# Performance work log

Measured on AMD Instinct MI355X. Metric: run time of the kernel, lower is better.

Reference implementation:

```python
import jax, jax.numpy as jnp
import numpy as np

NEG_SLOPE = 0.01  # torch nn.LeakyReLU default


def setup_inputs() -> dict:
    key = jax.random.key(0)
    k1, k2, k3, k4 = jax.random.split(key, 4)
    N, D = 8192, 64
    x = jax.random.normal(k1, (N, D), dtype=jnp.float32)
    W = jax.random.normal(k2, (D, D), dtype=jnp.float32) * (1.0 / np.sqrt(D))
    b = jax.random.normal(k3, (D,), dtype=jnp.float32) * 0.01
    a = jax.random.normal(k4, (2 * D, 1), dtype=jnp.float32)
    return {"x": x, "W": W, "b": b, "a": a}


def reference(x, W, b, a):
    # h = Linear(x): torch stores weight as [out, in], y = x @ W.T + b
    h = x @ W.T + b  # [N, D]
    D = h.shape[1]
    a1 = a[:D, 0]   # weights on the column node (e_x[i,j] = x_j)
    a2 = a[D:, 0]   # weights on the row node    (e_y[i,j] = x_i)
    s1 = h @ a1     # [N], contribution of node j
    s2 = h @ a2     # [N], contribution of node i
    # score[i, j] = a1.h_j + a2.h_i  (equivalent to expand+concat+matmul)
    scores = s2[:, None] + s1[None, :]                       # [N, N]
    scores = jnp.where(scores >= 0, scores, NEG_SLOPE * scores)  # leaky_relu
    att = jax.nn.softmax(scores, axis=1)                     # softmax over j
    # NOTE: forward multiplies attention with the ORIGINAL x, not h
    return att @ x                                           # [N, D]
```

## Files before the change

### kernel.cpp

```cpp
#include <hip/hip_runtime.h>

#define NEG_SLOPE 0.01f
#define LOG2E 1.4426950408889634f

constexpr int N = 8192;
constexpr int D = 64;
constexpr int PB = 32;
constexpr int RB = 32;
constexpr int NW = 8;

typedef __bf16 bf16x8 __attribute__((ext_vector_type(8)));
typedef float f32x4 __attribute__((ext_vector_type(4)));

#if __has_builtin(__builtin_amdgcn_exp2f)
#define EXP2(x) __builtin_amdgcn_exp2f(x)
#else
#define EXP2(x) exp2f(x)
#endif

__global__ __launch_bounds__(256) void gat_prep(
    const float* __restrict__ x, const float* __restrict__ W_,
    const float* __restrict__ b, const float* __restrict__ a,
    float* __restrict__ s1g, float* __restrict__ s2g,
    float* __restrict__ blockmax, bf16x8* __restrict__ xf) {
  __shared__ float w1s[D], w2s[D], cs[2];
  __shared__ float s1loc[PB];

  const int t = threadIdx.x;
  const int bid = blockIdx.x;

  if (t < 128) {
    const int sel = t >> 6, d = t & 63;
    const float* av = a + sel * D;
    float acc = 0.f;
#pragma unroll
    for (int k = 0; k < D; ++k) acc += W_[k * D + d] * av[k];
    (sel ? w2s : w1s)[d] = acc * LOG2E;
  }
  if (t == 128 || t == 129) {
    const int sel = t - 128;
    float acc = 0.f;
    for (int d = 0; d < D; ++d) acc += b[d] * a[sel * D + d];
    cs[sel] = acc * LOG2E;
  }
  __syncthreads();

  {
    const int r = t >> 3, seg = t & 7;
    const int gi = bid * PB + r;
    const float4 xa = *(const float4*)(x + (size_t)gi * D + seg * 8);
    const float4 xb = *(const float4*)(x + (size_t)gi * D + seg * 8 + 4);
    float p1 = xa.x * w1s[seg * 8 + 0] + xa.y * w1s[seg * 8 + 1] +
               xa.z * w1s[seg * 8 + 2] + xa.w * w1s[seg * 8 + 3] +
               xb.x * w1s[seg * 8 + 4] + xb.y * w1s[seg * 8 + 5] +
               xb.z * w1s[seg * 8 + 6] + xb.w * w1s[seg * 8 + 7];
    float p2 = xa.x * w2s[seg * 8 + 0] + xa.y * w2s[seg * 8 + 1] +
               xa.z * w2s[seg * 8 + 2] + xa.w * w2s[seg * 8 + 3] +
               xb.x * w2s[seg * 8 + 4] + xb.y * w2s[seg * 8 + 5] +
               xb.z * w2s[seg * 8 + 6] + xb.w * w2s[seg * 8 + 7];
#pragma unroll
    for (int off = 4; off; off >>= 1) {
      p1 += __shfl_xor(p1, off, 64);
      p2 += __shfl_xor(p2, off, 64);
    }
    if (seg == 0) {
      const float v1 = p1 + cs[0], v2 = p2 + cs[1];
      s1g[gi] = v1;
      s2g[gi] = v2;
      s1loc[r] = v1;
    }
  }

  {
    const int dt = t >> 6, fl = t & 63;
    const int jb = bid * PB + ((fl >> 4) << 3);
    const int col = dt * 16 + (fl & 15);
    bf16x8 f;
#pragma unroll
    for (int q = 0; q < 8; ++q) f[q] = (__bf16)x[(size_t)(jb + q) * D + col];
    xf[(bid << 8) | (dt << 6) | fl] = f;
  }
  __syncthreads();
  if (t == 0) {
    float m = s1loc[0];
#pragma unroll
    for (int r = 1; r < PB; ++r) m = fmaxf(m, s1loc[r]);
    blockmax[bid] = m;
  }
}

__global__ __launch_bounds__(512, 2) void gat_main(
    const bf16x8* __restrict__ xf, const float* __restrict__ s1g,
    const float* __restrict__ s2g, const float* __restrict__ blockmax,
    float* __restrict__ out) {
  __shared__ float accT[NW][RB][64];
  __shared__ float zt[NW][RB];
  __shared__ float gms;

  const int t = threadIdx.x;
  const int lane = t & 63;
  const int w = t >> 6;
  const int arow = lane & 15;
  const int grp = lane >> 4;
  const int ibase = blockIdx.x * RB;

  if (t < 64) {
    float v = fmaxf(fmaxf(blockmax[lane], blockmax[lane + 64]),
                    fmaxf(blockmax[lane + 128], blockmax[lane + 192]));
#pragma unroll
    for (int off = 32; off; off >>= 1) v = fmaxf(v, __shfl_xor(v, off, 64));
    if (lane == 0) gms = v;
  }
  __syncthreads();
  const float gm = gms;

  const float s2v0 = s2g[ibase + arow];
  const float s2v1 = s2g[ibase + 16 + arow];
  const float tm0 = s2v0 + gm, tm1 = s2v1 + gm;
  const float mneg0 = -fmaxf(tm0, NEG_SLOPE * tm0);
  const float mneg1 = -fmaxf(tm1, NEG_SLOPE * tm1);

  f32x4 a00 = {0.f, 0.f, 0.f, 0.f}, a01 = a00, a02 = a00, a03 = a00;
  f32x4 a10 = a00, a11 = a00, a12 = a00, a13 = a00;
  f32x4 az0 = a00, az1 = a00;
  bf16x8 ones;
#pragma unroll
  for (int q = 0; q < 8; ++q) ones[q] = (__bf16)1.0f;

  int c = w;
  bf16x8 xb0 = xf[(c << 8) + 0 * 64 + lane];
  bf16x8 xb1 = xf[(c << 8) + 1 * 64 + lane];
  bf16x8 xb2 = xf[(c << 8) + 2 * 64 + lane];
  bf16x8 xb3 = xf[(c << 8) + 3 * 64 + lane];
  float4 sa = *(const float4*)(s1g + c * 32 + grp * 8);
  float4 sb = *(const float4*)(s1g + c * 32 + grp * 8 + 4);

  constexpr int ITERS = N / 32 / NW;
  for (int i = 0; i < ITERS; ++i) {
    const int cn = (i == ITERS - 1) ? c : c + NW;
    bf16x8 nb0 = xf[(cn << 8) + 0 * 64 + lane];
    bf16x8 nb1 = xf[(cn << 8) + 1 * 64 + lane];
    bf16x8 nb2 = xf[(cn << 8) + 2 * 64 + lane];
    bf16x8 nb3 = xf[(cn << 8) + 3 * 64 + lane];
    const float4 na = *(const float4*)(s1g + cn * 32 + grp * 8);
    const float4 nbb = *(const float4*)(s1g + cn * 32 + grp * 8 + 4);

    bf16x8 pa0, pa1;
    {
      const float* sv = &sa.x;
#pragma unroll
      for (int q = 0; q < 4; ++q) {
        const float t0 = s2v0 + sv[q];
        pa0[q] = (__bf16)EXP2(fmaxf(t0, NEG_SLOPE * t0) + mneg0);
        const float t1 = s2v1 + sv[q];
        pa1[q] = (__bf16)EXP2(fmaxf(t1, NEG_SLOPE * t1) + mneg1);
      }
      const float* sw = &sb.x;
#pragma unroll
      for (int q = 0; q < 4; ++q) {
        const float t0 = s2v0 + sw[q];
        pa0[4 + q] = (__bf16)EXP2(fmaxf(t0, NEG_SLOPE * t0) + mneg0);
        const float t1 = s2v1 + sw[q];
        pa1[4 + q] = (__bf16)EXP2(fmaxf(t1, NEG_SLOPE * t1) + mneg1);
      }
    }

    a00 = __builtin_amdgcn_mfma_f32_16x16x32_bf16(pa0, xb0, a00, 0, 0, 0);
    a01 = __builtin_amdgcn_mfma_f32_16x16x32_bf16(pa0, xb1, a01, 0, 0, 0);
    a02 = __builtin_amdgcn_mfma_f32_16x16x32_bf16(pa0, xb2, a02, 0, 0, 0);
    a03 = __builtin_amdgcn_mfma_f32_16x16x32_bf16(pa0, xb3, a03, 0, 0, 0);
    az0 = __builtin_amdgcn_mfma_f32_16x16x32_bf16(pa0, ones, az0, 0, 0, 0);
    a10 = __builtin_amdgcn_mfma_f32_16x16x32_bf16(pa1, xb0, a10, 0, 0, 0);
    a11 = __builtin_amdgcn_mfma_f32_16x16x32_bf16(pa1, xb1, a11, 0, 0, 0);
    a12 = __builtin_amdgcn_mfma_f32_16x16x32_bf16(pa1, xb2, a12, 0, 0, 0);
    a13 = __builtin_amdgcn_mfma_f32_16x16x32_bf16(pa1, xb3, a13, 0, 0, 0);
    az1 = __builtin_amdgcn_mfma_f32_16x16x32_bf16(pa1, ones, az1, 0, 0, 0);

    xb0 = nb0; xb1 = nb1; xb2 = nb2; xb3 = nb3;
    sa = na; sb = nbb;
    c += NW;
  }

  if (arow == 0) {
#pragma unroll
    for (int reg = 0; reg < 4; ++reg) {
      zt[w][grp * 4 + reg] = az0[reg];
      zt[w][16 + grp * 4 + reg] = az1[reg];
    }
  }

#pragma unroll
  for (int reg = 0; reg < 4; ++reg) {
    accT[w][grp * 4 + reg][0 * 16 + arow] = a00[reg];
    accT[w][grp * 4 + reg][1 * 16 + arow] = a01[reg];
    accT[w][grp * 4 + reg][2 * 16 + arow] = a02[reg];
    accT[w][grp * 4 + reg][3 * 16 + arow] = a03[reg];
    accT[w][16 + grp * 4 + reg][0 * 16 + arow] = a10[reg];
    accT[w][16 + grp * 4 + reg][1 * 16 + arow] = a11[reg];
    accT[w][16 + grp * 4 + reg][2 * 16 + arow] = a12[reg];
    accT[w][16 + grp * 4 + reg][3 * 16 + arow] = a13[reg];
  }
  __syncthreads();

#pragma unroll
  for (int k = 0; k < 4; ++k) {
    const int r = w * 4 + k;
    float s = 0.f, z = 0.f;
#pragma unroll
    for (int v = 0; v < NW; ++v) {
      s += accT[v][r][lane];
      z += zt[v][r];
    }
    out[(size_t)(ibase + r) * D + lane] = s / z;
  }
}

extern "C" void kernel_launch(void* const* d_in, const int* in_sizes, int n_in,
                              void* d_out, int out_size, void* d_ws, size_t ws_size,
                              hipStream_t stream) {
  const float* x = (const float*)d_in[0];
  const float* W = (const float*)d_in[1];
  const float* b = (const float*)d_in[2];
  const float* a = (const float*)d_in[3];

  float* s1 = (float*)d_ws;
  float* s2 = s1 + N;
  float* blockmax = s2 + N;
  bf16x8* xf = (bf16x8*)((char*)d_ws + (1u << 20));
  float* out = (float*)d_out;

  gat_prep<<<N / PB, 256, 0, stream>>>(x, W, b, a, s1, s2, blockmax, xf);
  gat_main<<<N / RB, 512, 0, stream>>>(xf, s1, s2, blockmax, out);
}
```

Baseline: 91.60 us.

## Fuse prep and main kernels into one, recomputing scores per block

Merges the two kernels into a single launch. Every block recomputes all N s1 scores into shared memory (32KB) and its own s2 rows, then takes the global max locally. The main loop now reads fp32 x directly with strided scalar loads and converts to bf16 in registers, instead of reading a prepacked bf16 layout. This removes a launch and the workspace round trip, but each of the 256 blocks redundantly reads all of x (2MB) for the score pass. It also adds register pressure from the 64-float prefetch buffers, uncoalesced loads and more shared memory per block.

```diff
diff --git a/kernel.cpp b/kernel.cpp
--- a/kernel.cpp
+++ b/kernel.cpp
@@ -5,29 +5,27 @@
 
 constexpr int N = 8192;
 constexpr int D = 64;
-constexpr int PB = 32;
 constexpr int RB = 32;
 constexpr int NW = 8;
 
 typedef __bf16 bf16x8 __attribute__((ext_vector_type(8)));
 typedef float f32x4 __attribute__((ext_vector_type(4)));
 
-#if __has_builtin(__builtin_amdgcn_exp2f)
-#define EXP2(x) __builtin_amdgcn_exp2f(x)
-#else
-#define EXP2(x) exp2f(x)
-#endif
-
-__global__ __launch_bounds__(256) void gat_prep(
+__global__ __launch_bounds__(512, 2) void gat_one(
     const float* __restrict__ x, const float* __restrict__ W_,
     const float* __restrict__ b, const float* __restrict__ a,
-    float* __restrict__ s1g, float* __restrict__ s2g,
-    float* __restrict__ blockmax, bf16x8* __restrict__ xf) {
+    float* __restrict__ out) {
   __shared__ float w1s[D], w2s[D], cs[2];
-  __shared__ float s1loc[PB];
+  __shared__ float s1All[N];
+  __shared__ float s2loc[RB];
+  __shared__ float wmax[NW];
+  __shared__ float accT[NW][RB][64];
+  __shared__ float zt[NW][RB];
 
   const int t = threadIdx.x;
   const int bid = blockIdx.x;
+  const int lane = t & 63;
+  const int w = t >> 6;
 
   if (t < 128) {
     const int sel = t >> 6, d = t & 63;
@@ -46,76 +44,53 @@
   __syncthreads();
 
   {
-    const int r = t >> 3, seg = t & 7;
-    const int gi = bid * PB + r;
-    const float4 xa = *(const float4*)(x + (size_t)gi * D + seg * 8);
-    const float4 xb = *(const float4*)(x + (size_t)gi * D + seg * 8 + 4);
-    float p1 = xa.x * w1s[seg * 8 + 0] + xa.y * w1s[seg * 8 + 1] +
-               xa.z * w1s[seg * 8 + 2] + xa.w * w1s[seg * 8 + 3] +
-               xb.x * w1s[seg * 8 + 4] + xb.y * w1s[seg * 8 + 5] +
-               xb.z * w1s[seg * 8 + 6] + xb.w * w1s[seg * 8 + 7];
-    float p2 = xa.x * w2s[seg * 8 + 0] + xa.y * w2s[seg * 8 + 1] +
-               xa.z * w2s[seg * 8 + 2] + xa.w * w2s[seg * 8 + 3] +
-               xb.x * w2s[seg * 8 + 4] + xb.y * w2s[seg * 8 + 5] +
-               xb.z * w2s[seg * 8 + 6] + xb.w * w2s[seg * 8 + 7];
-#pragma unroll
-    for (int off = 4; off; off >>= 1) {
-      p1 += __shfl_xor(p1, off, 64);
-      p2 += __shfl_xor(p2, off, 64);
-    }
-    if (seg == 0) {
-      const float v1 = p1 + cs[0], v2 = p2 + cs[1];
-      s1g[gi] = v1;
-      s2g[gi] = v2;
-      s1loc[r] = v1;
-    }
-  }
-
+    const int seg = t & 7;
+    const int rloc = t >> 3;
+    float w1r[8], w2r[8];
+#pragma unroll
+    for (int k = 0; k < 8; ++k) { w1r[k] = w1s[seg * 8 + k]; w2r[k] = w2s[seg * 8 + k]; }
+    const float c1 = cs[0], c2 = cs[1];
+#pragma unroll 4
+    for (int it = 0; it < N / 64; ++it) {
+      const int gi = it * 64 + rloc;
+      const float4 xa = *(const float4*)(x + (size_t)gi * D + seg * 8);
+      const float4 xb = *(const float4*)(x + (size_t)gi * D + seg * 8 + 4);
+      float p1 = xa.x * w1r[0] + xa.y * w1r[1] + xa.z * w1r[2] + xa.w * w1r[3] +
+                 xb.x * w1r[4] + xb.y * w1r[5] + xb.z * w1r[6] + xb.w * w1r[7];
+      float p2 = xa.x * w2r[0] + xa.y * w2r[1] + xa.z * w2r[2] + xa.w * w2r[3] +
+                 xb.x * w2r[4] + xb.y * w2r[5] + xb.z * w2r[6] + xb.w * w2r[7];
+#pragma unroll
+      for (int off = 1; off < 8; off <<= 1) {
+        p1 += __shfl_xor(p1, off, 64);
+        p2 += __shfl_xor(p2, off, 64);
+      }
+      if (seg == 0) {
+        s1All[gi] = p1 + c1;
+        const int rown = gi - bid * RB;
+        if ((unsigned)rown < (unsigned)RB) s2loc[rown] = p2 + c2;
+      }
+    }
+  }
+  __syncthreads();
+
+  float gm;
   {
-    const int dt = t >> 6, fl = t & 63;
-    const int jb = bid * PB + ((fl >> 4) << 3);
-    const int col = dt * 16 + (fl & 15);
-    bf16x8 f;
-#pragma unroll
-    for (int q = 0; q < 8; ++q) f[q] = (__bf16)x[(size_t)(jb + q) * D + col];
-    xf[(bid << 8) | (dt << 6) | fl] = f;
-  }
-  __syncthreads();
-  if (t == 0) {
-    float m = s1loc[0];
-#pragma unroll
-    for (int r = 1; r < PB; ++r) m = fmaxf(m, s1loc[r]);
-    blockmax[bid] = m;
-  }
-}
-
-__global__ __launch_bounds__(512, 2) void gat_main(
-    const bf16x8* __restrict__ xf, const float* __restrict__ s1g,
-    const float* __restrict__ s2g, const float* __restrict__ blockmax,
-    float* __restrict__ out) {
-  __shared__ float accT[NW][RB][64];
-  __shared__ float zt[NW][RB];
-  __shared__ float gms;
-
-  const int t = threadIdx.x;
-  const int lane = t & 63;
-  const int w = t >> 6;
+    float mv = -1e30f;
+#pragma unroll
+    for (int k = 0; k < N / 512; ++k) mv = fmaxf(mv, s1All[k * 512 + t]);
+#pragma unroll
+    for (int off = 32; off; off >>= 1) mv = fmaxf(mv, __shfl_xor(mv, off, 64));
+    if (lane == 0) wmax[w] = mv;
+    __syncthreads();
+    gm = wmax[0];
+#pragma unroll
+    for (int k = 1; k < NW; ++k) gm = fmaxf(gm, wmax[k]);
+  }
+
   const int arow = lane & 15;
   const int grp = lane >> 4;
-  const int ibase = blockIdx.x * RB;
-
-  if (t < 64) {
-    float v = fmaxf(fmaxf(blockmax[lane], blockmax[lane + 64]),
-                    fmaxf(blockmax[lane + 128], blockmax[lane + 192]));
-#pragma unroll
-    for (int off = 32; off; off >>= 1) v = fmaxf(v, __shfl_xor(v, off, 64));
-    if (lane == 0) gms = v;
-  }
-  __syncthreads();
-  const float gm = gms;
-
-  const float s2v0 = s2g[ibase + arow];
-  const float s2v1 = s2g[ibase + 16 + arow];
+  const float s2v0 = s2loc[arow];
+  const float s2v1 = s2loc[16 + arow];
   const float tm0 = s2v0 + gm, tm1 = s2v1 + gm;
   const float mneg0 = -fmaxf(tm0, NEG_SLOPE * tm0);
   const float mneg1 = -fmaxf(tm1, NEG_SLOPE * tm1);
@@ -127,23 +102,42 @@
 #pragma unroll
   for (int q = 0; q < 8; ++q) ones[q] = (__bf16)1.0f;
 
+  float xc[32], xn[32];
+  float4 sa, sb, na, nb;
+  {
+    const float* bp = x + (size_t)w * 2048 + grp * 512 + arow;
+#pragma unroll
+    for (int q = 0; q < 8; ++q)
+#pragma unroll
+      for (int dt = 0; dt < 4; ++dt) xc[q * 4 + dt] = bp[q * 64 + dt * 16];
+    const float* sp = &s1All[w * 32 + grp * 8];
+    sa = *(const float4*)sp;
+    sb = *(const float4*)(sp + 4);
+  }
+
+  constexpr int ITERS = N / 32 / NW;
   int c = w;
-  bf16x8 xb0 = xf[(c << 8) + 0 * 64 + lane];
-  bf16x8 xb1 = xf[(c << 8) + 1 * 64 + lane];
-  bf16x8 xb2 = xf[(c << 8) + 2 * 64 + lane];
-  bf16x8 xb3 = xf[(c << 8) + 3 * 64 + lane];
-  float4 sa = *(const float4*)(s1g + c * 32 + grp * 8);
-  float4 sb = *(const float4*)(s1g + c * 32 + grp * 8 + 4);
-
-  constexpr int ITERS = N / 32 / NW;
   for (int i = 0; i < ITERS; ++i) {
     const int cn = (i == ITERS - 1) ? c : c + NW;
-    bf16x8 nb0 = xf[(cn << 8) + 0 * 64 + lane];
-    bf16x8 nb1 = xf[(cn << 8) + 1 * 64 + lane];
-    bf16x8 nb2 = xf[(cn << 8) + 2 * 64 + lane];
-    bf16x8 nb3 = xf[(cn << 8) + 3 * 64 + lane];
-    const float4 na = *(const float4*)(s1g + cn * 32 + grp * 8);
-    const float4 nbb = *(const float4*)(s1g + cn * 32 + grp * 8 + 4);
+    {
+      const float* bp = x + (size_t)cn * 2048 + grp * 512 + arow;
+#pragma unroll
+      for (int q = 0; q < 8; ++q)
+#pragma unroll
+        for (int dt = 0; dt < 4; ++dt) xn[q * 4 + dt] = bp[q * 64 + dt * 16];
+      const float* sp = &s1All[cn * 32 + grp * 8];
+      na = *(const float4*)sp;
+      nb = *(const float4*)(sp + 4);
+    }
+
+    bf16x8 xb0, xb1, xb2, xb3;
+#pragma unroll
+    for (int q = 0; q < 8; ++q) {
+      xb0[q] = (__bf16)xc[q * 4 + 0];
+      xb1[q] = (__bf16)xc[q * 4 + 1];
+      xb2[q] = (__bf16)xc[q * 4 + 2];
+      xb3[q] = (__bf16)xc[q * 4 + 3];
+    }
 
     bf16x8 pa0, pa1;
     {
@@ -151,17 +145,17 @@
 #pragma unroll
       for (int q = 0; q < 4; ++q) {
         const float t0 = s2v0 + sv[q];
-        pa0[q] = (__bf16)EXP2(fmaxf(t0, NEG_SLOPE * t0) + mneg0);
+        pa0[q] = (__bf16)exp2f(fmaxf(t0, NEG_SLOPE * t0) + mneg0);
         const float t1 = s2v1 + sv[q];
-        pa1[q] = (__bf16)EXP2(fmaxf(t1, NEG_SLOPE * t1) + mneg1);
+        pa1[q] = (__bf16)exp2f(fmaxf(t1, NEG_SLOPE * t1) + mneg1);
       }
       const float* sw = &sb.x;
 #pragma unroll
       for (int q = 0; q < 4; ++q) {
         const float t0 = s2v0 + sw[q];
-        pa0[4 + q] = (__bf16)EXP2(fmaxf(t0, NEG_SLOPE * t0) + mneg0);
+        pa0[4 + q] = (__bf16)exp2f(fmaxf(t0, NEG_SLOPE * t0) + mneg0);
         const float t1 = s2v1 + sw[q];
-        pa1[4 + q] = (__bf16)EXP2(fmaxf(t1, NEG_SLOPE * t1) + mneg1);
+        pa1[4 + q] = (__bf16)exp2f(fmaxf(t1, NEG_SLOPE * t1) + mneg1);
       }
     }
 
@@ -176,8 +170,9 @@
     a13 = __builtin_amdgcn_mfma_f32_16x16x32_bf16(pa1, xb3, a13, 0, 0, 0);
     az1 = __builtin_amdgcn_mfma_f32_16x16x32_bf16(pa1, ones, az1, 0, 0, 0);
 
-    xb0 = nb0; xb1 = nb1; xb2 = nb2; xb3 = nb3;
-    sa = na; sb = nbb;
+#pragma unroll
+    for (int q = 0; q < 32; ++q) xc[q] = xn[q];
+    sa = na; sb = nb;
     c += NW;
   }
 
@@ -188,7 +183,6 @@
       zt[w][16 + grp * 4 + reg] = az1[reg];
     }
   }
-
 #pragma unroll
   for (int reg = 0; reg < 4; ++reg) {
     accT[w][grp * 4 + reg][0 * 16 + arow] = a00[reg];
@@ -211,7 +205,7 @@
       s += accT[v][r][lane];
       z += zt[v][r];
     }
-    out[(size_t)(ibase + r) * D + lane] = s / z;
+    out[(size_t)(bid * RB + r) * D + lane] = s / z;
   }
 }
 
@@ -222,13 +216,7 @@
   const float* W = (const float*)d_in[1];
   const float* b = (const float*)d_in[2];
   const float* a = (const float*)d_in[3];
-
-  float* s1 = (float*)d_ws;
-  float* s2 = s1 + N;
-  float* blockmax = s2 + N;
-  bf16x8* xf = (bf16x8*)((char*)d_ws + (1u << 20));
   float* out = (float*)d_out;
 
-  gat_prep<<<N / PB, 256, 0, stream>>>(x, W, b, a, s1, s2, blockmax, xf);
-  gat_main<<<N / RB, 512, 0, stream>>>(xf, s1, s2, blockmax, out);
+  gat_one<<<N / RB, 512, 0, stream>>>(x, W, b, a, out);
 }
```

New measurement: 150.6 us. 64.4% more time.

## Stage s1 in LDS, double-buffer x fragments, and fold leaky-relu constants

Applied to the files above, without the earlier changes.

The main kernel now copies the whole s1 vector into shared memory at startup, so inner-loop score reads come from LDS instead of global memory. The bf16 x fragments are prefetched two iterations ahead using two register sets, which gives the loads more time to land before use. The leaky-relu plus max-subtraction is rewritten as fmax of two affine forms with precomputed per-row constants, removing a few ALU ops per exp. The accumulator transpose buffer is padded to 65 columns to avoid bank conflicts; the trade-off is a 32KB+ LDS footprint that may reduce occupancy and more registers for the double buffer.

```diff
diff --git a/kernel.cpp b/kernel.cpp
--- a/kernel.cpp
+++ b/kernel.cpp
@@ -93,7 +93,8 @@
     const bf16x8* __restrict__ xf, const float* __restrict__ s1g,
     const float* __restrict__ s2g, const float* __restrict__ blockmax,
     float* __restrict__ out) {
-  __shared__ float accT[NW][RB][64];
+  __shared__ float s1s[N];
+  __shared__ float accT[NW][RB][65];
   __shared__ float zt[NW][RB];
   __shared__ float gms;
 
@@ -104,6 +105,10 @@
   const int grp = lane >> 4;
   const int ibase = blockIdx.x * RB;
 
+#pragma unroll
+  for (int k = 0; k < N / 4 / 512; ++k)
+    ((float4*)s1s)[k * 512 + t] = ((const float4*)s1g)[k * 512 + t];
+
   if (t < 64) {
     float v = fmaxf(fmaxf(blockmax[lane], blockmax[lane + 64]),
                     fmaxf(blockmax[lane + 128], blockmax[lane + 192]));
@@ -119,6 +124,8 @@
   const float tm0 = s2v0 + gm, tm1 = s2v1 + gm;
   const float mneg0 = -fmaxf(tm0, NEG_SLOPE * tm0);
   const float mneg1 = -fmaxf(tm1, NEG_SLOPE * tm1);
+  const float A0 = s2v0 + mneg0, B0 = fmaf(NEG_SLOPE, s2v0, mneg0);
+  const float A1 = s2v1 + mneg1, B1 = fmaf(NEG_SLOPE, s2v1, mneg1);
 
   f32x4 a00 = {0.f, 0.f, 0.f, 0.f}, a01 = a00, a02 = a00, a03 = a00;
   f32x4 a10 = a00, a11 = a00, a12 = a00, a13 = a00;
@@ -127,58 +134,65 @@
 #pragma unroll
   for (int q = 0; q < 8; ++q) ones[q] = (__bf16)1.0f;
 
-  int c = w;
-  bf16x8 xb0 = xf[(c << 8) + 0 * 64 + lane];
-  bf16x8 xb1 = xf[(c << 8) + 1 * 64 + lane];
-  bf16x8 xb2 = xf[(c << 8) + 2 * 64 + lane];
-  bf16x8 xb3 = xf[(c << 8) + 3 * 64 + lane];
-  float4 sa = *(const float4*)(s1g + c * 32 + grp * 8);
-  float4 sb = *(const float4*)(s1g + c * 32 + grp * 8 + 4);
-
-  constexpr int ITERS = N / 32 / NW;
-  for (int i = 0; i < ITERS; ++i) {
-    const int cn = (i == ITERS - 1) ? c : c + NW;
-    bf16x8 nb0 = xf[(cn << 8) + 0 * 64 + lane];
-    bf16x8 nb1 = xf[(cn << 8) + 1 * 64 + lane];
-    bf16x8 nb2 = xf[(cn << 8) + 2 * 64 + lane];
-    bf16x8 nb3 = xf[(cn << 8) + 3 * 64 + lane];
-    const float4 na = *(const float4*)(s1g + cn * 32 + grp * 8);
-    const float4 nbb = *(const float4*)(s1g + cn * 32 + grp * 8 + 4);
-
+  bf16x8 pA0, pA1, pA2, pA3, pB0, pB1, pB2, pB3;
+  {
+    const int fa = w << 8;
+    pA0 = xf[fa + 0 * 64 + lane]; pA1 = xf[fa + 1 * 64 + lane];
+    pA2 = xf[fa + 2 * 64 + lane]; pA3 = xf[fa + 3 * 64 + lane];
+    const int fb = (w + NW) << 8;
+    pB0 = xf[fb + 0 * 64 + lane]; pB1 = xf[fb + 1 * 64 + lane];
+    pB2 = xf[fb + 2 * 64 + lane]; pB3 = xf[fb + 3 * 64 + lane];
+  }
+
+  auto process = [&](const bf16x8& x0, const bf16x8& x1, const bf16x8& x2,
+                     const bf16x8& x3, int c) {
+    const float4 sa = *(const float4*)&s1s[c * 32 + grp * 8];
+    const float4 sb = *(const float4*)&s1s[c * 32 + grp * 8 + 4];
     bf16x8 pa0, pa1;
+    const float* sv = &sa.x;
+#pragma unroll
+    for (int q = 0; q < 4; ++q) {
+      const float s = sv[q];
+      pa0[q] = (__bf16)EXP2(fmaxf(s + A0, fmaf(NEG_SLOPE, s, B0)));
+      pa1[q] = (__bf16)EXP2(fmaxf(s + A1, fmaf(NEG_SLOPE, s, B1)));
+    }
+    const float* sw = &sb.x;
+#pragma unroll
+    for (int q = 0; q < 4; ++q) {
+      const float s = sw[q];
+      pa0[4 + q] = (__bf16)EXP2(fmaxf(s + A0, fmaf(NEG_SLOPE, s, B0)));
+      pa1[4 + q] = (__bf16)EXP2(fmaxf(s + A1, fmaf(NEG_SLOPE, s, B1)));
+    }
+    a00 = __builtin_amdgcn_mfma_f32_16x16x32_bf16(pa0, x0, a00, 0, 0, 0);
+    a01 = __builtin_amdgcn_mfma_f32_16x16x32_bf16(pa0, x1, a01, 0, 0, 0);
+    a02 = __builtin_amdgcn_mfma_f32_16x16x32_bf16(pa0, x2, a02, 0, 0, 0);
+    a03 = __builtin_amdgcn_mfma_f32_16x16x32_bf16(pa0, x3, a03, 0, 0, 0);
+    az0 = __builtin_amdgcn_mfma_f32_16x16x32_bf16(pa0, ones, az0, 0, 0, 0);
+    a10 = __builtin_amdgcn_mfma_f32_16x16x32_bf16(pa1, x0, a10, 0, 0, 0);
+    a11 = __builtin_amdgcn_mfma_f32_16x16x32_bf16(pa1, x1, a11, 0, 0, 0);
+    a12 = __builtin_amdgcn_mfma_f32_16x16x32_bf16(pa1, x2, a12, 0, 0, 0);
+    a13 = __builtin_amdgcn_mfma_f32_16x16x32_bf16(pa1, x3, a13, 0, 0, 0);
+    az1 = __builtin_amdgcn_mfma_f32_16x16x32_bf16(pa1, ones, az1, 0, 0, 0);
+  };
+
+  int c0 = w;
+  constexpr int PAIRS = N / 32 / NW / 2;
+  for (int i = 0; i < PAIRS; ++i) {
+    process(pA0, pA1, pA2, pA3, c0);
     {
-      const float* sv = &sa.x;
-#pragma unroll
-      for (int q = 0; q < 4; ++q) {
-        const float t0 = s2v0 + sv[q];
-        pa0[q] = (__bf16)EXP2(fmaxf(t0, NEG_SLOPE * t0) + mneg0);
-        const float t1 = s2v1 + sv[q];
-        pa1[q] = (__bf16)EXP2(fmaxf(t1, NEG_SLOPE * t1) + mneg1);
-      }
-      const float* sw = &sb.x;
-#pragma unroll
-      for (int q = 0; q < 4; ++q) {
-        const float t0 = s2v0 + sw[q];
-        pa0[4 + q] = (__bf16)EXP2(fmaxf(t0, NEG_SLOPE * t0) + mneg0);
-        const float t1 = s2v1 + sw[q];
-        pa1[4 + q] = (__bf16)EXP2(fmaxf(t1, NEG_SLOPE * t1) + mneg1);
-      }
-    }
-
-    a00 = __builtin_amdgcn_mfma_f32_16x16x32_bf16(pa0, xb0, a00, 0, 0, 0);
-    a01 = __builtin_amdgcn_mfma_f32_16x16x32_bf16(pa0, xb1, a01, 0, 0, 0);
-    a02 = __builtin_amdgcn_mfma_f32_16x16x32_bf16(pa0, xb2, a02, 0, 0, 0);
-    a03 = __builtin_amdgcn_mfma_f32_16x16x32_bf16(pa0, xb3, a03, 0, 0, 0);
-    az0 = __builtin_amdgcn_mfma_f32_16x16x32_bf16(pa0, ones, az0, 0, 0, 0);
-    a10 = __builtin_amdgcn_mfma_f32_16x16x32_bf16(pa1, xb0, a10, 0, 0, 0);
-    a11 = __builtin_amdgcn_mfma_f32_16x16x32_bf16(pa1, xb1, a11, 0, 0, 0);
-    a12 = __builtin_amdgcn_mfma_f32_16x16x32_bf16(pa1, xb2, a12, 0, 0, 0);
-    a13 = __builtin_amdgcn_mfma_f32_16x16x32_bf16(pa1, xb3, a13, 0, 0, 0);
-    az1 = __builtin_amdgcn_mfma_f32_16x16x32_bf16(pa1, ones, az1, 0, 0, 0);
-
-    xb0 = nb0; xb1 = nb1; xb2 = nb2; xb3 = nb3;
-    sa = na; sb = nbb;
-    c += NW;
+      const int cn = (i == PAIRS - 1) ? c0 : c0 + 2 * NW;
+      const int f = cn << 8;
+      pA0 = xf[f + 0 * 64 + lane]; pA1 = xf[f + 1 * 64 + lane];
+      pA2 = xf[f + 2 * 64 + lane]; pA3 = xf[f + 3 * 64 + lane];
+    }
+    process(pB0, pB1, pB2, pB3, c0 + NW);
+    {
+      const int cn = (i == PAIRS - 1) ? c0 + NW : c0 + 3 * NW;
+      const int f = cn << 8;
+      pB0 = xf[f + 0 * 64 + lane]; pB1 = xf[f + 1 * 64 + lane];
+      pB2 = xf[f + 2 * 64 + lane]; pB3 = xf[f + 3 * 64 + lane];
+    }
+    c0 += 2 * NW;
   }
 
   if (arow == 0) {
@@ -188,7 +202,6 @@
       zt[w][16 + grp * 4 + reg] = az1[reg];
     }
   }
-
 #pragma unroll
   for (int reg = 0; reg < 4; ++reg) {
     accT[w][grp * 4 + reg][0 * 16 + arow] = a00[reg];
```

Result: faster. 83.75 us (-8.6%).
